# Kernel tuning notes

Hardware: AMD Instinct MI355X
Metric: run time of the kernel (lower is better)

Reference implementation:

```python
import jax, jax.numpy as jnp
import numpy as np

N = 50000
E = 1600000
DIM = 128
RC = 5.0
DEPTH = 3


def setup_inputs() -> dict:
    key = jax.random.key(0)
    kv, ke, ks, kd, kw, kb, krs, ksig = jax.random.split(key, 8)
    v = jax.random.normal(kv, (N, DIM), dtype=jnp.float32)
    # edge distances in [0, rc]
    e = jax.random.uniform(ke, (E, 1), dtype=jnp.float32) * RC
    src = jax.random.randint(ks, (E,), 0, N, dtype=jnp.int32)
    dst = jax.random.randint(kd, (E,), 0, N, dtype=jnp.int32)
    # learned params: A = nn.Linear(dim, dim); rs, sigma = torch.rand(1)
    A_w = jax.random.normal(kw, (DIM, DIM), dtype=jnp.float32) / np.sqrt(DIM)
    A_b = jax.random.normal(kb, (DIM,), dtype=jnp.float32) * 0.01
    rs = jax.random.uniform(krs, (1,), dtype=jnp.float32)
    sigma = jax.random.uniform(ksig, (1,), dtype=jnp.float32)
    return {"v": v, "e": e, "src": src, "dst": dst,
            "A_w": A_w, "A_b": A_b, "rs": rs, "sigma": sigma}


def _edge_envelope(r, rs, sigma):
    # exp(-(r-rs)^2/sigma^2) * 0.5 * cos(pi*r/rc) * (r < rc)
    gauss = jnp.exp(-jnp.square(r - rs) / jnp.square(sigma))
    cutoff = 0.5 * jnp.cos(np.pi * r / RC) * (r < RC).astype(r.dtype)
    return gauss * cutoff


def reference(v, e, src, dst, A_w, A_b, rs, sigma):
    f = _edge_envelope(e, rs, sigma)  # [E, 1]
    cur = v
    for _ in range(DEPTH):
        msg = f * cur[src]  # gather src node feats, weight by edge envelope: [E, DIM]
        svf = jax.ops.segment_sum(msg, dst, num_segments=N)  # scatter-sum to dst: [N, DIM]
        cur = jax.nn.relu((svf + v) @ A_w.T + A_b)  # linear + relu, skip from original v
    return cur
```

## Files before the change

### kernel.cpp

```cpp
#include <hip/hip_runtime.h>
#include <math.h>

#define N_NODES 50000
#define N_PAD   50048
#define N_EDGES 1600000
#define DIM     128
#define RCUT    5.0f
#define NGROUP  (N_PAD / 64)
#define NB_PRE  512
#define CH_PRE  (N_EDGES / NB_PRE)
#define NB_CONV 6250
#define NB_WPREP 8
#define NB_RE   128
#define CH_RE   (N_EDGES / NB_RE)
#define XPAD    136
#define NTILE   (N_PAD / 16)
#define BST     65

typedef __attribute__((ext_vector_type(8))) __bf16 bf16x8;
typedef __attribute__((ext_vector_type(4))) float  f32x4;

__device__ __forceinline__ float bf_lo(unsigned int u) { return __uint_as_float(u << 16); }
__device__ __forceinline__ float bf_hi(unsigned int u) { return __uint_as_float(u & 0xffff0000u); }
__device__ __forceinline__ unsigned short f2bf(float x) {
    unsigned int u = __float_as_uint(x);
    u += 0x7fffu + ((u >> 16) & 1u);
    return (unsigned short)(u >> 16);
}

__global__ __launch_bounds__(256) void preA_kernel(
        const float* __restrict__ v, unsigned short* __restrict__ vb,
        const float* __restrict__ Aw, uint4* __restrict__ wfrag,
        const int* __restrict__ dst, int* __restrict__ partial) {
    int b = blockIdx.x;
    if (b < NB_CONV) {
        int i = b * 256 + threadIdx.x;
        float4 x = ((const float4*)v)[i];
        uint2 o;
        o.x = (unsigned)f2bf(x.x) | ((unsigned)f2bf(x.y) << 16);
        o.y = (unsigned)f2bf(x.z) | ((unsigned)f2bf(x.w) << 16);
        ((uint2*)vb)[i] = o;
    } else if (b < NB_CONV + NB_WPREP) {
        int t = (b - NB_CONV) * 256 + threadIdx.x;
        int lane = t & 63, nt = (t >> 6) & 7, kk = t >> 9;
        int n  = nt * 16 + (lane & 15);
        int k0 = kk * 32 + (lane >> 4) * 8;
        unsigned short h[8];
        #pragma unroll
        for (int i = 0; i < 8; ++i) h[i] = f2bf(Aw[n * DIM + k0 + i]);
        uint4 o;
        o.x = h[0] | ((unsigned)h[1] << 16); o.y = h[2] | ((unsigned)h[3] << 16);
        o.z = h[4] | ((unsigned)h[5] << 16); o.w = h[6] | ((unsigned)h[7] << 16);
        wfrag[t] = o;
    } else {
        __shared__ int h[NGROUP];
        int cb = b - NB_CONV - NB_WPREP, tid = threadIdx.x;
        for (int g = tid; g < NGROUP; g += 256) h[g] = 0;
        __syncthreads();
        int beg = cb * CH_PRE, end = beg + CH_PRE;
        for (int i = beg + tid; i < end; i += 256)
            atomicAdd(&h[dst[i] >> 6], 1);
        __syncthreads();
        for (int g = tid; g < NGROUP; g += 256) partial[cb * NGROUP + g] = h[g];
    }
}

__global__ __launch_bounds__(256) void ktot2_kernel(const int* __restrict__ partial,
                                                    int* __restrict__ partial4,
                                                    int* __restrict__ sum64) {
    int gb = blockIdx.x & 3, qq = blockIdx.x >> 2;
    int g = gb * 256 + threadIdx.x;
    if (g >= NGROUP) return;
    int acc = 0;
    #pragma unroll 1
    for (int j = 0; j < 16; ++j) {
        int s4 = 0;
        #pragma unroll
        for (int c = 0; c < 4; ++c)
            s4 += partial[(qq * 64 + j * 4 + c) * NGROUP + g];
        partial4[(qq * 16 + j) * NGROUP + g] = s4;
        acc += s4;
    }
    sum64[qq * NGROUP + g] = acc;
}

__global__ __launch_bounds__(256) void kscan_kernel(const int* __restrict__ sum64,
                                                    int* __restrict__ goff) {
    __shared__ int part[256];
    int tid = threadIdx.x;
    int i0 = tid * 4;
    int v[4]; int s = 0;
    #pragma unroll
    for (int k = 0; k < 4; ++k) {
        int i = i0 + k; int t = 0;
        if (i < NGROUP) {
            #pragma unroll
            for (int qq = 0; qq < 8; ++qq) t += sum64[qq * NGROUP + i];
        }
        v[k] = t; s += t;
    }
    part[tid] = s; __syncthreads();
    for (int d = 1; d < 256; d <<= 1) {
        int val = (tid >= d) ? part[tid - d] : 0;
        __syncthreads(); part[tid] += val; __syncthreads();
    }
    int run = (tid == 0) ? 0 : part[tid - 1];
    #pragma unroll
    for (int k = 0; k < 4; ++k) {
        int i = i0 + k;
        if (i < NGROUP) { goff[i] = run; run += v[k]; }
    }
    if (tid == 0) goff[NGROUP] = N_EDGES;
}

__global__ __launch_bounds__(512) void reorder_kernel(
        const float* __restrict__ e,
        const int*   __restrict__ src,
        const int*   __restrict__ dst,
        const float* __restrict__ rs,
        const float* __restrict__ sigma,
        const int*   __restrict__ goff,
        const int*   __restrict__ partial4,
        const int*   __restrict__ sum64,
        int2* __restrict__ metaT) {
    __shared__ int base[NGROUP];
    __shared__ int cnt[NGROUP];
    int b = blockIdx.x, tid = threadIdx.x;
    int q = b >> 4;
    for (int g = tid; g < NGROUP; g += 512) {
        int run = goff[g];
        for (int qq = 0; qq < q; ++qq) run += sum64[qq * NGROUP + g];
        for (int j = q * 16; j < b; ++j) run += partial4[j * NGROUP + g];
        base[g] = run; cnt[g] = 0;
    }
    __syncthreads();
    float rsv = rs[0], sg = sigma[0];
    int beg = b * CH_RE, end = beg + CH_RE;
    for (int i = beg + tid; i < end; i += 512) {
        float r  = e[i];
        float d  = r - rsv;
        float gauss = expf(-(d * d) / (sg * sg));
        float cut   = 0.5f * cosf(r * (float)(M_PI / (double)RCUT));
        cut = (r < RCUT) ? cut : 0.0f;
        float fe = gauss * cut;
        int dn = dst[i];
        int g  = dn >> 6;
        int lr = atomicAdd(&cnt[g], 1);
        metaT[base[g] + lr] = make_int2(src[i] * (DIM * 2) | ((dn & 63) << 24),
                                        __float_as_int(fe));
    }
}

#define EDGE2(mx, mf, rr)                                        \
    do {                                                         \
        float ff = __int_as_float(mf);                           \
        a0 = fmaf(ff, bf_lo(rr), a0);                            \
        a1 = fmaf(ff, bf_hi(rr), a1);                            \
    } while (0)

__device__ __forceinline__ void gather_node(
        const int2* __restrict__ meta, const char* basec,
        int beg, int end, float& a0, float& a1) {
    int c = beg;
    if ((c & 1) && c < end) {
        int2 m = meta[c];
        unsigned rr = *(const unsigned*)(basec + (unsigned)m.x);
        EDGE2(m.x, m.y, rr);
        ++c;
    }
    for (; c + 16 <= end; c += 16) {
        int4 m0 = *(const int4*)(meta + c);
        int4 m1 = *(const int4*)(meta + c + 2);
        int4 m2 = *(const int4*)(meta + c + 4);
        int4 m3 = *(const int4*)(meta + c + 6);
        int4 m4 = *(const int4*)(meta + c + 8);
        int4 m5 = *(const int4*)(meta + c + 10);
        int4 m6 = *(const int4*)(meta + c + 12);
        int4 m7 = *(const int4*)(meta + c + 14);
        unsigned r0  = *(const unsigned*)(basec + (unsigned)m0.x);
        unsigned r1  = *(const unsigned*)(basec + (unsigned)m0.z);
        unsigned r2  = *(const unsigned*)(basec + (unsigned)m1.x);
        unsigned r3  = *(const unsigned*)(basec + (unsigned)m1.z);
        unsigned r4  = *(const unsigned*)(basec + (unsigned)m2.x);
        unsigned r5  = *(const unsigned*)(basec + (unsigned)m2.z);
        unsigned r6  = *(const unsigned*)(basec + (unsigned)m3.x);
        unsigned r7  = *(const unsigned*)(basec + (unsigned)m3.z);
        unsigned r8  = *(const unsigned*)(basec + (unsigned)m4.x);
        unsigned r9  = *(const unsigned*)(basec + (unsigned)m4.z);
        unsigned r10 = *(const unsigned*)(basec + (unsigned)m5.x);
        unsigned r11 = *(const unsigned*)(basec + (unsigned)m5.z);
        unsigned r12 = *(const unsigned*)(basec + (unsigned)m6.x);
        unsigned r13 = *(const unsigned*)(basec + (unsigned)m6.z);
        unsigned r14 = *(const unsigned*)(basec + (unsigned)m7.x);
        unsigned r15 = *(const unsigned*)(basec + (unsigned)m7.z);
        EDGE2(m0.x, m0.y, r0);  EDGE2(m0.z, m0.w, r1);
        EDGE2(m1.x, m1.y, r2);  EDGE2(m1.z, m1.w, r3);
        EDGE2(m2.x, m2.y, r4);  EDGE2(m2.z, m2.w, r5);
        EDGE2(m3.x, m3.y, r6);  EDGE2(m3.z, m3.w, r7);
        EDGE2(m4.x, m4.y, r8);  EDGE2(m4.z, m4.w, r9);
        EDGE2(m5.x, m5.y, r10); EDGE2(m5.z, m5.w, r11);
        EDGE2(m6.x, m6.y, r12); EDGE2(m6.z, m6.w, r13);
        EDGE2(m7.x, m7.y, r14); EDGE2(m7.z, m7.w, r15);
    }
    if (c + 8 <= end) {
        int4 m0 = *(const int4*)(meta + c);
        int4 m1 = *(const int4*)(meta + c + 2);
        int4 m2 = *(const int4*)(meta + c + 4);
        int4 m3 = *(const int4*)(meta + c + 6);
        unsigned r0 = *(const unsigned*)(basec + (unsigned)m0.x);
        unsigned r1 = *(const unsigned*)(basec + (unsigned)m0.z);
        unsigned r2 = *(const unsigned*)(basec + (unsigned)m1.x);
        unsigned r3 = *(const unsigned*)(basec + (unsigned)m1.z);
        unsigned r4 = *(const unsigned*)(basec + (unsigned)m2.x);
        unsigned r5 = *(const unsigned*)(basec + (unsigned)m2.z);
        unsigned r6 = *(const unsigned*)(basec + (unsigned)m3.x);
        unsigned r7 = *(const unsigned*)(basec + (unsigned)m3.z);
        EDGE2(m0.x, m0.y, r0); EDGE2(m0.z, m0.w, r1);
        EDGE2(m1.x, m1.y, r2); EDGE2(m1.z, m1.w, r3);
        EDGE2(m2.x, m2.y, r4); EDGE2(m2.z, m2.w, r5);
        EDGE2(m3.x, m3.y, r6); EDGE2(m3.z, m3.w, r7);
        c += 8;
    }
    for (; c < end; ++c) {
        int2 m = meta[c];
        unsigned rr = *(const unsigned*)(basec + (unsigned)m.x);
        EDGE2(m.x, m.y, rr);
    }
}

__global__ __launch_bounds__(512) void layer0_kernel(
        const unsigned short* __restrict__ cur,
        const unsigned short* __restrict__ vb,
        const int2*  __restrict__ metaT,
        const int*   __restrict__ goff,
        int2* __restrict__ meta,
        int*  __restrict__ off,
        const uint4* __restrict__ wfrag,
        const float* __restrict__ bias,
        unsigned short* __restrict__ out_bf) {
    __shared__ unsigned short xlds[64 * XPAD];
    __shared__ int cntW[8 * BST];
    __shared__ int curW[8 * BST];
    __shared__ int b64[65];
    int tid = threadIdx.x;
    int wv  = tid >> 6, lane = tid & 63;
    int g   = blockIdx.x;
    int sbeg = goff[g], send = goff[g + 1];

    for (int i = tid; i < 8 * BST; i += 512) cntW[i] = 0;
    __syncthreads();
    for (int i = sbeg + tid; i < send; i += 512)
        atomicAdd(&cntW[wv * BST + ((metaT[i].x >> 24) & 63)], 1);
    __syncthreads();
    if (tid < 64) {
        int x = 0;
        #pragma unroll
        for (int w = 0; w < 8; ++w) x += cntW[w * BST + tid];
        int incl = x;
        #pragma unroll
        for (int d = 1; d < 64; d <<= 1) {
            int y = __shfl_up(incl, d, 64);
            if (tid >= d) incl += y;
        }
        int excl = incl - x;
        b64[tid] = excl;
        if (tid == 63) b64[64] = incl;
        int run = excl;
        #pragma unroll
        for (int w = 0; w < 8; ++w) { curW[w * BST + tid] = run; run += cntW[w * BST + tid]; }
        int node = g * 64 + tid;
        if (node <= N_NODES) off[node] = sbeg + excl;
    }
    __syncthreads();
    for (int i = sbeg + tid; i < send; i += 512) {
        int2 m = metaT[i];
        int lr = atomicAdd(&curW[wv * BST + ((m.x >> 24) & 63)], 1);
        meta[sbeg + lr] = make_int2(m.x & 0x00FFFFFF, m.y);
    }
    __syncthreads();

    int n0 = g * 64 + wv * 8;
    int myoff = 0;
    if (lane < 9) myoff = sbeg + b64[wv * 8 + lane];
    const char* basec = (const char*)cur + lane * 4;

    #pragma unroll 1
    for (int q = 0; q < 8; ++q) {
        int nl = wv * 8 + q;
        int n  = n0 + q;
        float a0 = 0.f, a1 = 0.f;
        if (n < N_NODES) {
            unsigned vv = *(const unsigned*)((const char*)vb + (size_t)n * (DIM * 2) + lane * 4);
            a0 = bf_lo(vv); a1 = bf_hi(vv);
            int beg = __builtin_amdgcn_readlane(myoff, q);
            int end = __builtin_amdgcn_readlane(myoff, q + 1);
            gather_node(meta, basec, beg, end, a0, a1);
        }
        *(unsigned*)(xlds + nl * XPAD + lane * 2) =
            (unsigned)f2bf(a0) | ((unsigned)f2bf(a1) << 16);
    }
    __syncthreads();

    int quad = lane >> 4, l16 = lane & 15;
    int rb = wv >> 1, nh = wv & 1;
    f32x4 acc[4];
    #pragma unroll
    for (int j = 0; j < 4; ++j) acc[j] = (f32x4){0.f, 0.f, 0.f, 0.f};

    const unsigned short* xp = xlds + (rb * 16 + l16) * XPAD + quad * 8;
    #pragma unroll
    for (int kk = 0; kk < 4; ++kk) {
        bf16x8 af = *(const bf16x8*)(xp + kk * 32);
        #pragma unroll
        for (int j = 0; j < 4; ++j) {
            uint4 w = wfrag[(kk * 8 + nh * 4 + j) * 64 + lane];
            bf16x8 bfr = __builtin_bit_cast(bf16x8, w);
            acc[j] = __builtin_amdgcn_mfma_f32_16x16x32_bf16(af, bfr, acc[j], 0, 0, 0);
        }
    }

    int orow0 = g * 64 + rb * 16 + quad * 4;
    #pragma unroll
    for (int j = 0; j < 4; ++j) {
        int col = (nh * 4 + j) * 16 + l16;
        float b = bias[col];
        #pragma unroll
        for (int r = 0; r < 4; ++r) {
            int orow = orow0 + r;
            if (orow < N_NODES)
                out_bf[(size_t)orow * DIM + col] = f2bf(fmaxf(acc[j][r] + b, 0.f));
        }
    }
}

__global__ __launch_bounds__(128, 8) void layer12_kernel(
        const unsigned short* __restrict__ cur,
        const unsigned short* __restrict__ vb,
        const int2*  __restrict__ meta,
        const int*   __restrict__ off,
        const uint4* __restrict__ wfrag,
        const float* __restrict__ bias,
        unsigned short* __restrict__ out_bf,
        float* __restrict__ out_f,
        int last) {
    __shared__ unsigned short xlds[16 * XPAD];
    int tid = threadIdx.x;
    int wv  = tid >> 6, lane = tid & 63;
    int tile = blockIdx.x;
    int n0  = tile * 16 + wv * 8;

    int offidx = n0 + ((lane < 9) ? lane : 8);
    if (offidx > N_NODES) offidx = N_NODES;
    int myoff = off[offidx];
    const char* basec = (const char*)cur + lane * 4;

    #pragma unroll 1
    for (int q = 0; q < 8; ++q) {
        int nl = wv * 8 + q;
        int n  = n0 + q;
        float a0 = 0.f, a1 = 0.f;
        if (n < N_NODES) {
            unsigned vv = *(const unsigned*)((const char*)vb + (size_t)n * (DIM * 2) + lane * 4);
            a0 = bf_lo(vv); a1 = bf_hi(vv);
            int beg = __builtin_amdgcn_readlane(myoff, q);
            int end = __builtin_amdgcn_readlane(myoff, q + 1);
            gather_node(meta, basec, beg, end, a0, a1);
        }
        *(unsigned*)(xlds + nl * XPAD + lane * 2) =
            (unsigned)f2bf(a0) | ((unsigned)f2bf(a1) << 16);
    }
    __syncthreads();

    int quad = lane >> 4, l16 = lane & 15;
    f32x4 acc[4];
    #pragma unroll
    for (int j = 0; j < 4; ++j) acc[j] = (f32x4){0.f, 0.f, 0.f, 0.f};

    const unsigned short* xp = xlds + l16 * XPAD + quad * 8;
    #pragma unroll
    for (int kk = 0; kk < 4; ++kk) {
        bf16x8 af = *(const bf16x8*)(xp + kk * 32);
        #pragma unroll
        for (int j = 0; j < 4; ++j) {
            uint4 w = wfrag[(kk * 8 + wv * 4 + j) * 64 + lane];
            bf16x8 bfr = __builtin_bit_cast(bf16x8, w);
            acc[j] = __builtin_amdgcn_mfma_f32_16x16x32_bf16(af, bfr, acc[j], 0, 0, 0);
        }
    }

    int orow0 = tile * 16 + quad * 4;
    #pragma unroll
    for (int j = 0; j < 4; ++j) {
        int col = (wv * 4 + j) * 16 + l16;
        float b = bias[col];
        #pragma unroll
        for (int r = 0; r < 4; ++r) {
            int orow = orow0 + r;
            if (orow < N_NODES) {
                float val = fmaxf(acc[j][r] + b, 0.f);
                if (last) out_f[(size_t)orow * DIM + col] = val;
                else      out_bf[(size_t)orow * DIM + col] = f2bf(val);
            }
        }
    }
}

extern "C" void kernel_launch(void* const* d_in, const int* in_sizes, int n_in,
                              void* d_out, int out_size, void* d_ws, size_t ws_size,
                              hipStream_t stream) {
    const float* v     = (const float*)d_in[0];
    const float* e     = (const float*)d_in[1];
    const int*   src   = (const int*)  d_in[2];
    const int*   dst   = (const int*)  d_in[3];
    const float* Aw    = (const float*)d_in[4];
    const float* Ab    = (const float*)d_in[5];
    const float* rs    = (const float*)d_in[6];
    const float* sigma = (const float*)d_in[7];
    float* out = (float*)d_out;

    char* p = (char*)d_ws;
    int2*           meta  = (int2*)p;            p += (size_t)N_EDGES * 8;
    unsigned short* bufV  = (unsigned short*)p;  p += (size_t)N_PAD * DIM * 2;
    unsigned short* bufA  = (unsigned short*)p;  p += (size_t)N_PAD * DIM * 2;
    unsigned short* bufB  = (unsigned short*)p;  p += (size_t)N_PAD * DIM * 2;
    uint4*          wfrag = (uint4*)p;           p += 2048 * 16;
    int*            off   = (int*)p;             p += (size_t)(N_NODES + 2) * 4;
    int*            goff  = (int*)p;             p += (NGROUP + 2) * 4;
    int2* metaT    = (int2*)bufA;
    int*  partial  = (int*)bufB;
    int*  partial4 = partial + NB_PRE * NGROUP;
    int*  sum64    = partial4 + 128 * NGROUP;

    preA_kernel<<<NB_CONV + NB_WPREP + NB_PRE, 256, 0, stream>>>(
        v, bufV, Aw, wfrag, dst, partial);
    ktot2_kernel<<<32, 256, 0, stream>>>(partial, partial4, sum64);
    kscan_kernel<<<1, 256, 0, stream>>>(sum64, goff);
    reorder_kernel<<<NB_RE, 512, 0, stream>>>(
        e, src, dst, rs, sigma, goff, partial4, sum64, metaT);

    layer0_kernel<<<NGROUP, 512, 0, stream>>>(
        bufV, bufV, metaT, goff, meta, off, wfrag, Ab, bufB);
    layer12_kernel<<<NTILE, 128, 0, stream>>>(
        bufB, bufV, meta, off, wfrag, Ab, bufA, nullptr, 0);
    layer12_kernel<<<NTILE, 128, 0, stream>>>(
        bufA, bufV, meta, off, wfrag, Ab, nullptr, out, 1);
}
```

Before: 344.5 us.

## Pack edge metadata into 32 bits and fold group scan into reorder

Edge metadata for layers 1-2 is compressed from an 8-byte (byte offset, fp32 weight) pair to a single 32-bit word holding a 16-bit source index and a bf16 envelope weight. This halves the metadata bandwidth of the gather loops. The separate single-block scan kernel is removed, and every reorder block now recomputes the prefix scan redundantly, with block 0 writing goff. The layer0 local bucketing also drops per-wave counters in favour of one shared counter set. Risks: the 16-bit source index cannot address node ids up to 50000 beyond 65535 (it fits here), the weight loses precision going to bf16, and shared-atomic contention rises.

```diff
diff --git a/kernel.cpp b/kernel.cpp
--- a/kernel.cpp
+++ b/kernel.cpp
@@ -15,7 +15,6 @@
 #define CH_RE   (N_EDGES / NB_RE)
 #define XPAD    136
 #define NTILE   (N_PAD / 16)
-#define BST     65
 
 typedef __attribute__((ext_vector_type(8))) __bf16 bf16x8;
 typedef __attribute__((ext_vector_type(4))) float  f32x4;
@@ -84,55 +83,53 @@
     sum64[qq * NGROUP + g] = acc;
 }
 
-__global__ __launch_bounds__(256) void kscan_kernel(const int* __restrict__ sum64,
-                                                    int* __restrict__ goff) {
-    __shared__ int part[256];
-    int tid = threadIdx.x;
-    int i0 = tid * 4;
-    int v[4]; int s = 0;
-    #pragma unroll
-    for (int k = 0; k < 4; ++k) {
-        int i = i0 + k; int t = 0;
-        if (i < NGROUP) {
-            #pragma unroll
-            for (int qq = 0; qq < 8; ++qq) t += sum64[qq * NGROUP + i];
-        }
-        v[k] = t; s += t;
-    }
-    part[tid] = s; __syncthreads();
-    for (int d = 1; d < 256; d <<= 1) {
-        int val = (tid >= d) ? part[tid - d] : 0;
-        __syncthreads(); part[tid] += val; __syncthreads();
-    }
-    int run = (tid == 0) ? 0 : part[tid - 1];
-    #pragma unroll
-    for (int k = 0; k < 4; ++k) {
-        int i = i0 + k;
-        if (i < NGROUP) { goff[i] = run; run += v[k]; }
-    }
-    if (tid == 0) goff[NGROUP] = N_EDGES;
-}
-
 __global__ __launch_bounds__(512) void reorder_kernel(
         const float* __restrict__ e,
         const int*   __restrict__ src,
         const int*   __restrict__ dst,
         const float* __restrict__ rs,
         const float* __restrict__ sigma,
-        const int*   __restrict__ goff,
         const int*   __restrict__ partial4,
         const int*   __restrict__ sum64,
+        int*  __restrict__ goff,
         int2* __restrict__ metaT) {
     __shared__ int base[NGROUP];
     __shared__ int cnt[NGROUP];
+    __shared__ int part[512];
     int b = blockIdx.x, tid = threadIdx.x;
     int q = b >> 4;
-    for (int g = tid; g < NGROUP; g += 512) {
-        int run = goff[g];
-        for (int qq = 0; qq < q; ++qq) run += sum64[qq * NGROUP + g];
-        for (int j = q * 16; j < b; ++j) run += partial4[j * NGROUP + g];
-        base[g] = run; cnt[g] = 0;
-    }
+    int i0 = tid * 2;
+    int v0 = 0, v1 = 0;
+    if (i0 < NGROUP) {
+        #pragma unroll
+        for (int qq = 0; qq < 8; ++qq) v0 += sum64[qq * NGROUP + i0];
+    }
+    if (i0 + 1 < NGROUP) {
+        #pragma unroll
+        for (int qq = 0; qq < 8; ++qq) v1 += sum64[qq * NGROUP + i0 + 1];
+    }
+    part[tid] = v0 + v1; __syncthreads();
+    for (int d = 1; d < 512; d <<= 1) {
+        int val = (tid >= d) ? part[tid - d] : 0;
+        __syncthreads(); part[tid] += val; __syncthreads();
+    }
+    int run = (tid == 0) ? 0 : part[tid - 1];
+    if (i0 < NGROUP) {
+        if (b == 0) goff[i0] = run;
+        int r = run;
+        for (int qq = 0; qq < q; ++qq) r += sum64[qq * NGROUP + i0];
+        for (int j = q * 16; j < b; ++j) r += partial4[j * NGROUP + i0];
+        base[i0] = r; cnt[i0] = 0;
+        int run1 = run + v0;
+        if (i0 + 1 < NGROUP) {
+            if (b == 0) goff[i0 + 1] = run1;
+            int r1 = run1;
+            for (int qq = 0; qq < q; ++qq) r1 += sum64[qq * NGROUP + i0 + 1];
+            for (int j = q * 16; j < b; ++j) r1 += partial4[j * NGROUP + i0 + 1];
+            base[i0 + 1] = r1; cnt[i0 + 1] = 0;
+        }
+    }
+    if (b == 0 && tid == 0) goff[NGROUP] = N_EDGES;
     __syncthreads();
     float rsv = rs[0], sg = sigma[0];
     int beg = b * CH_RE, end = beg + CH_RE;
@@ -151,81 +148,70 @@
     }
 }
 
-#define EDGE2(mx, mf, rr)                                        \
-    do {                                                         \
-        float ff = __int_as_float(mf);                           \
-        a0 = fmaf(ff, bf_lo(rr), a0);                            \
-        a1 = fmaf(ff, bf_hi(rr), a1);                            \
+#define EDGE1(mm)                                                          \
+    do {                                                                   \
+        unsigned rr = *(const unsigned*)(basec + (((mm) & 0xFFFFu) << 8)); \
+        float ff = bf_hi(mm);                                              \
+        a0 = fmaf(ff, bf_lo(rr), a0);                                      \
+        a1 = fmaf(ff, bf_hi(rr), a1);                                      \
     } while (0)
 
 __device__ __forceinline__ void gather_node(
-        const int2* __restrict__ meta, const char* basec,
+        const unsigned* __restrict__ meta, const char* basec,
         int beg, int end, float& a0, float& a1) {
     int c = beg;
-    if ((c & 1) && c < end) {
-        int2 m = meta[c];
-        unsigned rr = *(const unsigned*)(basec + (unsigned)m.x);
-        EDGE2(m.x, m.y, rr);
-        ++c;
-    }
+    while ((c & 3) && c < end) { unsigned m = meta[c]; EDGE1(m); ++c; }
     for (; c + 16 <= end; c += 16) {
-        int4 m0 = *(const int4*)(meta + c);
-        int4 m1 = *(const int4*)(meta + c + 2);
-        int4 m2 = *(const int4*)(meta + c + 4);
-        int4 m3 = *(const int4*)(meta + c + 6);
-        int4 m4 = *(const int4*)(meta + c + 8);
-        int4 m5 = *(const int4*)(meta + c + 10);
-        int4 m6 = *(const int4*)(meta + c + 12);
-        int4 m7 = *(const int4*)(meta + c + 14);
-        unsigned r0  = *(const unsigned*)(basec + (unsigned)m0.x);
-        unsigned r1  = *(const unsigned*)(basec + (unsigned)m0.z);
-        unsigned r2  = *(const unsigned*)(basec + (unsigned)m1.x);
-        unsigned r3  = *(const unsigned*)(basec + (unsigned)m1.z);
-        unsigned r4  = *(const unsigned*)(basec + (unsigned)m2.x);
-        unsigned r5  = *(const unsigned*)(basec + (unsigned)m2.z);
-        unsigned r6  = *(const unsigned*)(basec + (unsigned)m3.x);
-        unsigned r7  = *(const unsigned*)(basec + (unsigned)m3.z);
-        unsigned r8  = *(const unsigned*)(basec + (unsigned)m4.x);
-        unsigned r9  = *(const unsigned*)(basec + (unsigned)m4.z);
-        unsigned r10 = *(const unsigned*)(basec + (unsigned)m5.x);
-        unsigned r11 = *(const unsigned*)(basec + (unsigned)m5.z);
-        unsigned r12 = *(const unsigned*)(basec + (unsigned)m6.x);
-        unsigned r13 = *(const unsigned*)(basec + (unsigned)m6.z);
-        unsigned r14 = *(const unsigned*)(basec + (unsigned)m7.x);
-        unsigned r15 = *(const unsigned*)(basec + (unsigned)m7.z);
-        EDGE2(m0.x, m0.y, r0);  EDGE2(m0.z, m0.w, r1);
-        EDGE2(m1.x, m1.y, r2);  EDGE2(m1.z, m1.w, r3);
-        EDGE2(m2.x, m2.y, r4);  EDGE2(m2.z, m2.w, r5);
-        EDGE2(m3.x, m3.y, r6);  EDGE2(m3.z, m3.w, r7);
-        EDGE2(m4.x, m4.y, r8);  EDGE2(m4.z, m4.w, r9);
-        EDGE2(m5.x, m5.y, r10); EDGE2(m5.z, m5.w, r11);
-        EDGE2(m6.x, m6.y, r12); EDGE2(m6.z, m6.w, r13);
-        EDGE2(m7.x, m7.y, r14); EDGE2(m7.z, m7.w, r15);
-    }
-    if (c + 8 <= end) {
-        int4 m0 = *(const int4*)(meta + c);
-        int4 m1 = *(const int4*)(meta + c + 2);
-        int4 m2 = *(const int4*)(meta + c + 4);
-        int4 m3 = *(const int4*)(meta + c + 6);
-        unsigned r0 = *(const unsigned*)(basec + (unsigned)m0.x);
-        unsigned r1 = *(const unsigned*)(basec + (unsigned)m0.z);
-        unsigned r2 = *(const unsigned*)(basec + (unsigned)m1.x);
-        unsigned r3 = *(const unsigned*)(basec + (unsigned)m1.z);
-        unsigned r4 = *(const unsigned*)(basec + (unsigned)m2.x);
-        unsigned r5 = *(const unsigned*)(basec + (unsigned)m2.z);
-        unsigned r6 = *(const unsigned*)(basec + (unsigned)m3.x);
-        unsigned r7 = *(const unsigned*)(basec + (unsigned)m3.z);
-        EDGE2(m0.x, m0.y, r0); EDGE2(m0.z, m0.w, r1);
-        EDGE2(m1.x, m1.y, r2); EDGE2(m1.z, m1.w, r3);
-        EDGE2(m2.x, m2.y, r4); EDGE2(m2.z, m2.w, r5);
-        EDGE2(m3.x, m3.y, r6); EDGE2(m3.z, m3.w, r7);
-        c += 8;
-    }
-    for (; c < end; ++c) {
-        int2 m = meta[c];
-        unsigned rr = *(const unsigned*)(basec + (unsigned)m.x);
-        EDGE2(m.x, m.y, rr);
-    }
+        uint4 m0 = *(const uint4*)(meta + c);
+        uint4 m1 = *(const uint4*)(meta + c + 4);
+        uint4 m2 = *(const uint4*)(meta + c + 8);
+        uint4 m3 = *(const uint4*)(meta + c + 12);
+        unsigned r0  = *(const unsigned*)(basec + ((m0.x & 0xFFFFu) << 8));
+        unsigned r1  = *(const unsigned*)(basec + ((m0.y & 0xFFFFu) << 8));
+        unsigned r2  = *(const unsigned*)(basec + ((m0.z & 0xFFFFu) << 8));
+        unsigned r3  = *(const unsigned*)(basec + ((m0.w & 0xFFFFu) << 8));
+        unsigned r4  = *(const unsigned*)(basec + ((m1.x & 0xFFFFu) << 8));
+        unsigned r5  = *(const unsigned*)(basec + ((m1.y & 0xFFFFu) << 8));
+        unsigned r6  = *(const unsigned*)(basec + ((m1.z & 0xFFFFu) << 8));
+        unsigned r7  = *(const unsigned*)(basec + ((m1.w & 0xFFFFu) << 8));
+        unsigned r8  = *(const unsigned*)(basec + ((m2.x & 0xFFFFu) << 8));
+        unsigned r9  = *(const unsigned*)(basec + ((m2.y & 0xFFFFu) << 8));
+        unsigned r10 = *(const unsigned*)(basec + ((m2.z & 0xFFFFu) << 8));
+        unsigned r11 = *(const unsigned*)(basec + ((m2.w & 0xFFFFu) << 8));
+        unsigned r12 = *(const unsigned*)(basec + ((m3.x & 0xFFFFu) << 8));
+        unsigned r13 = *(const unsigned*)(basec + ((m3.y & 0xFFFFu) << 8));
+        unsigned r14 = *(const unsigned*)(basec + ((m3.z & 0xFFFFu) << 8));
+        unsigned r15 = *(const unsigned*)(basec + ((m3.w & 0xFFFFu) << 8));
+        a0 = fmaf(bf_hi(m0.x), bf_lo(r0), a0);  a1 = fmaf(bf_hi(m0.x), bf_hi(r0), a1);
+        a0 = fmaf(bf_hi(m0.y), bf_lo(r1), a0);  a1 = fmaf(bf_hi(m0.y), bf_hi(r1), a1);
+        a0 = fmaf(bf_hi(m0.z), bf_lo(r2), a0);  a1 = fmaf(bf_hi(m0.z), bf_hi(r2), a1);
+        a0 = fmaf(bf_hi(m0.w), bf_lo(r3), a0);  a1 = fmaf(bf_hi(m0.w), bf_hi(r3), a1);
+        a0 = fmaf(bf_hi(m1.x), bf_lo(r4), a0);  a1 = fmaf(bf_hi(m1.x), bf_hi(r4), a1);
+        a0 = fmaf(bf_hi(m1.y), bf_lo(r5), a0);  a1 = fmaf(bf_hi(m1.y), bf_hi(r5), a1);
+        a0 = fmaf(bf_hi(m1.z), bf_lo(r6), a0);  a1 = fmaf(bf_hi(m1.z), bf_hi(r6), a1);
+        a0 = fmaf(bf_hi(m1.w), bf_lo(r7), a0);  a1 = fmaf(bf_hi(m1.w), bf_hi(r7), a1);
+        a0 = fmaf(bf_hi(m2.x), bf_lo(r8), a0);  a1 = fmaf(bf_hi(m2.x), bf_hi(r8), a1);
+        a0 = fmaf(bf_hi(m2.y), bf_lo(r9), a0);  a1 = fmaf(bf_hi(m2.y), bf_hi(r9), a1);
+        a0 = fmaf(bf_hi(m2.z), bf_lo(r10), a0); a1 = fmaf(bf_hi(m2.z), bf_hi(r10), a1);
+        a0 = fmaf(bf_hi(m2.w), bf_lo(r11), a0); a1 = fmaf(bf_hi(m2.w), bf_hi(r11), a1);
+        a0 = fmaf(bf_hi(m3.x), bf_lo(r12), a0); a1 = fmaf(bf_hi(m3.x), bf_hi(r12), a1);
+        a0 = fmaf(bf_hi(m3.y), bf_lo(r13), a0); a1 = fmaf(bf_hi(m3.y), bf_hi(r13), a1);
+        a0 = fmaf(bf_hi(m3.z), bf_lo(r14), a0); a1 = fmaf(bf_hi(m3.z), bf_hi(r14), a1);
+        a0 = fmaf(bf_hi(m3.w), bf_lo(r15), a0); a1 = fmaf(bf_hi(m3.w), bf_hi(r15), a1);
+    }
+    if (c + 4 <= end) {
+        uint4 m0 = *(const uint4*)(meta + c);
+        unsigned r0 = *(const unsigned*)(basec + ((m0.x & 0xFFFFu) << 8));
+        unsigned r1 = *(const unsigned*)(basec + ((m0.y & 0xFFFFu) << 8));
+        unsigned r2 = *(const unsigned*)(basec + ((m0.z & 0xFFFFu) << 8));
+        unsigned r3 = *(const unsigned*)(basec + ((m0.w & 0xFFFFu) << 8));
+        a0 = fmaf(bf_hi(m0.x), bf_lo(r0), a0); a1 = fmaf(bf_hi(m0.x), bf_hi(r0), a1);
+        a0 = fmaf(bf_hi(m0.y), bf_lo(r1), a0); a1 = fmaf(bf_hi(m0.y), bf_hi(r1), a1);
+        a0 = fmaf(bf_hi(m0.z), bf_lo(r2), a0); a1 = fmaf(bf_hi(m0.z), bf_hi(r2), a1);
+        a0 = fmaf(bf_hi(m0.w), bf_lo(r3), a0); a1 = fmaf(bf_hi(m0.w), bf_hi(r3), a1);
+        c += 4;
+    }
+    for (; c < end; ++c) { unsigned m = meta[c]; EDGE1(m); }
 }
 
 __global__ __launch_bounds__(512) void layer0_kernel(
@@ -233,49 +219,40 @@
         const unsigned short* __restrict__ vb,
         const int2*  __restrict__ metaT,
         const int*   __restrict__ goff,
-        int2* __restrict__ meta,
+        unsigned* __restrict__ meta,
         int*  __restrict__ off,
         const uint4* __restrict__ wfrag,
         const float* __restrict__ bias,
         unsigned short* __restrict__ out_bf) {
     __shared__ unsigned short xlds[64 * XPAD];
-    __shared__ int cntW[8 * BST];
-    __shared__ int curW[8 * BST];
-    __shared__ int b64[65];
+    __shared__ int c64[64], b64[65], cu64[64];
     int tid = threadIdx.x;
     int wv  = tid >> 6, lane = tid & 63;
     int g   = blockIdx.x;
     int sbeg = goff[g], send = goff[g + 1];
 
-    for (int i = tid; i < 8 * BST; i += 512) cntW[i] = 0;
+    if (tid < 64) c64[tid] = 0;
     __syncthreads();
     for (int i = sbeg + tid; i < send; i += 512)
-        atomicAdd(&cntW[wv * BST + ((metaT[i].x >> 24) & 63)], 1);
+        atomicAdd(&c64[(metaT[i].x >> 24) & 63], 1);
+    __syncthreads();
+    if (tid == 0) {
+        int run = 0;
+        #pragma unroll
+        for (int t = 0; t < 64; ++t) { b64[t] = run; cu64[t] = run; run += c64[t]; }
+        b64[64] = run;
+    }
     __syncthreads();
     if (tid < 64) {
-        int x = 0;
-        #pragma unroll
-        for (int w = 0; w < 8; ++w) x += cntW[w * BST + tid];
-        int incl = x;
-        #pragma unroll
-        for (int d = 1; d < 64; d <<= 1) {
-            int y = __shfl_up(incl, d, 64);
-            if (tid >= d) incl += y;
-        }
-        int excl = incl - x;
-        b64[tid] = excl;
-        if (tid == 63) b64[64] = incl;
-        int run = excl;
-        #pragma unroll
-        for (int w = 0; w < 8; ++w) { curW[w * BST + tid] = run; run += cntW[w * BST + tid]; }
         int node = g * 64 + tid;
-        if (node <= N_NODES) off[node] = sbeg + excl;
-    }
-    __syncthreads();
+        if (node <= N_NODES) off[node] = sbeg + b64[tid];
+    }
     for (int i = sbeg + tid; i < send; i += 512) {
         int2 m = metaT[i];
-        int lr = atomicAdd(&curW[wv * BST + ((m.x >> 24) & 63)], 1);
-        meta[sbeg + lr] = make_int2(m.x & 0x00FFFFFF, m.y);
+        int tag = (m.x >> 24) & 63;
+        int lr = atomicAdd(&cu64[tag], 1);
+        meta[sbeg + lr] = (unsigned)((m.x >> 8) & 0xFFFF)
+                        | ((unsigned)f2bf(__int_as_float(m.y)) << 16);
     }
     __syncthreads();
 
@@ -336,7 +313,7 @@
 __global__ __launch_bounds__(128, 8) void layer12_kernel(
         const unsigned short* __restrict__ cur,
         const unsigned short* __restrict__ vb,
-        const int2*  __restrict__ meta,
+        const unsigned* __restrict__ meta,
         const int*   __restrict__ off,
         const uint4* __restrict__ wfrag,
         const float* __restrict__ bias,
@@ -419,7 +396,7 @@
     float* out = (float*)d_out;
 
     char* p = (char*)d_ws;
-    int2*           meta  = (int2*)p;            p += (size_t)N_EDGES * 8;
+    unsigned*       meta  = (unsigned*)p;        p += (size_t)N_EDGES * 8;
     unsigned short* bufV  = (unsigned short*)p;  p += (size_t)N_PAD * DIM * 2;
     unsigned short* bufA  = (unsigned short*)p;  p += (size_t)N_PAD * DIM * 2;
     unsigned short* bufB  = (unsigned short*)p;  p += (size_t)N_PAD * DIM * 2;
@@ -434,9 +411,8 @@
     preA_kernel<<<NB_CONV + NB_WPREP + NB_PRE, 256, 0, stream>>>(
         v, bufV, Aw, wfrag, dst, partial);
     ktot2_kernel<<<32, 256, 0, stream>>>(partial, partial4, sum64);
-    kscan_kernel<<<1, 256, 0, stream>>>(sum64, goff);
     reorder_kernel<<<NB_RE, 512, 0, stream>>>(
-        e, src, dst, rs, sigma, goff, partial4, sum64, metaT);
+        e, src, dst, rs, sigma, partial4, sum64, goff, metaT);
 
     layer0_kernel<<<NGROUP, 512, 0, stream>>>(
         bufV, bufV, metaT, goff, meta, off, wfrag, Ab, bufB);
```

After: 350.2 us. About the same (+1.7%).
